# Kernel tuning notes

Measured on AMD Instinct MI355X. Metric: run time of the kernel, lower is better.

Reference implementation:

```python
import jax, jax.numpy as jnp
import numpy as np

B, V, D, K, C_IN, C_OUT = 64, 2000, 16, 3, 64, 64


def setup_inputs() -> dict:
    key = jax.random.key(0)
    ks = jax.random.split(key, 7)
    return {
        "x": jax.random.normal(ks[0], (B, V, C_IN), dtype=jnp.float32),
        "ne_re": jax.random.normal(ks[1], (V, D), dtype=jnp.float32),
        "ne_im": jax.random.normal(ks[2], (V, D), dtype=jnp.float32),
        "w_re": jax.random.normal(ks[3], (D, K, C_IN, C_OUT), dtype=jnp.float32),
        "w_im": jax.random.normal(ks[4], (D, K, C_IN, C_OUT), dtype=jnp.float32),
        "b_re": jax.random.normal(ks[5], (D, C_OUT), dtype=jnp.float32),
        "b_im": jax.random.normal(ks[6], (D, C_OUT), dtype=jnp.float32),
    }


def reference(x, ne_re, ne_im, w_re, w_im, b_re, b_im):
    # Complex node embeddings and parameter pools (param_type='complex').
    ne = jax.lax.complex(ne_re, ne_im)                      # (V, D) complex64
    w_pool = jax.lax.complex(w_re, w_im)                    # (D, K, Ci, Co)
    b_pool = jax.lax.complex(b_re, b_im)                    # (D, Co)

    # Laplacian = E E^H, Frobenius-normalized (activation=None, normalization='frob').
    lap = ne @ ne.conj().T                                  # (V, V)
    lap = lap / jnp.linalg.norm(lap)

    # Node-adaptive weights and bias.
    weights = jnp.einsum('vd,dkio->vkio', ne, w_pool)       # (V, K, Ci, Co)
    bias = ne @ b_pool                                      # (V, Co)

    # Chebyshev-style recurrence, faithful to the source: T_k = 2*T_{k-1} - T_{k-2}
    # (the original code omits the laplacian matmul in the recurrence).
    polys = [jnp.eye(V, dtype=lap.dtype), lap]
    for k in range(2, K):
        polys.append(2.0 * polys[k - 1] - polys[k - 2])
    cheb = jnp.stack(polys, axis=0)                         # (K, V, V)

    xc = x.astype(lap.dtype)                                # (B, V, Ci)
    gx = jnp.einsum('kuv,bvi->buki', cheb, xc)              # (B, V, K, Ci)
    out = jnp.einsum('bvki,vkio->bvo', gx, weights) + bias  # (B, V, Co) complex

    # unwind=True path: view_as_real + flatten(2,3) -> interleaved (re, im).
    return jnp.stack([out.real, out.imag], axis=-1).reshape(B, V, 2 * C_OUT)
```

## Files before the change

### kernel.cpp

```cpp
#include <hip/hip_runtime.h>
#include <stdint.h>

#define BB 64
#define VV 2000
#define DD 16
#define CI 64
#define CO 64

#define WS_INV_DW   0
#define WS_Z_DW     1024
#define WS_BIAS_DW  132096
#define WS_NE_B     1552384UL
#define WS_RHS_B    1814528UL
#define WS_U_B      4960256UL
#define WS_W_B      54112256UL
#define WS_ZP_DW    33554432
#define WS_NP_DW    (WS_ZP_DW + 2097152)

typedef __attribute__((ext_vector_type(8))) short short8;
typedef __attribute__((ext_vector_type(4))) float f32x4;

__device__ __forceinline__ uint32_t f2bf(float f) {
  uint32_t u = __float_as_uint(f);
  return (u + 0x7FFFu + ((u >> 16) & 1u)) >> 16;
}

__device__ __forceinline__ void gload_lds16(const void* g, void* l) {
  __builtin_amdgcn_global_load_lds(
      (const __attribute__((address_space(1))) uint32_t*)g,
      (__attribute__((address_space(3))) uint32_t*)l, 16, 0, 0);
}


__device__ __forceinline__ void body_z(int bz, int t,
    const float* __restrict__ x, const float* __restrict__ ne_re,
    const float* __restrict__ ne_im, float* __restrict__ ws) {
  int b = bz >> 4, c = bz & 15;
  int lane = t & 63;
  int w = __builtin_amdgcn_readfirstlane(t >> 6);
  __shared__ __align__(16) float smem[8192];

  int vbase = c * 125;

  {
    const float4* xg = (const float4*)(x + ((size_t)b * VV + vbase) * CI);
    int wb = t & 192;
    #pragma unroll
    for (int p = 0; p < 8; ++p) {
      int idx = p * 256 + t;
      if (idx < 2000)
        gload_lds16(xg + idx, &smem[(p * 256 + wb) * 4]);
    }
  }
  __syncthreads();

  float zr[DD], zi[DD];
  #pragma unroll
  for (int d = 0; d < DD; ++d) { zr[d] = 0.f; zi[d] = 0.f; }

  uint16_t* Ux = (uint16_t*)((char*)ws + WS_U_B);
  int bkey = b & 7;
  int pos = (((lane >> 3) ^ bkey) & 7)*8 + (lane & 7);

  int lv0 = (w * 125) >> 2;
  int lv1 = ((w + 1) * 125) >> 2;
  #pragma unroll 4
  for (int lv = lv0; lv < lv1; ++lv) {
    float xv = smem[lv * 64 + lane];
    int v = vbase + lv;
    Ux[(size_t)v*12288 + b*64 + pos] = (uint16_t)f2bf(xv);
    #pragma unroll
    for (int d = 0; d < DD; ++d) {
      zr[d] += ne_re[v*DD + d] * xv;
      zi[d] -= ne_im[v*DD + d] * xv;
    }
  }
  __syncthreads();

  #pragma unroll
  for (int d = 0; d < DD; ++d) {
    smem[w*2048 + d*128 + lane*2 + 0] = zr[d];
    smem[w*2048 + d*128 + lane*2 + 1] = zi[d];
  }
  __syncthreads();
  float* ZP = ws + WS_ZP_DW;
  #pragma unroll
  for (int k = 0; k < 8; ++k) {
    int j = t + k*256;
    float s = smem[j] + smem[2048 + j] + smem[4096 + j] + smem[6144 + j];
    int d = j >> 7, r = j & 127;
    ZP[(size_t)c*131072 + d*8192 + b*128 + r] = s;
  }
}

__device__ __forceinline__ void body_ne(int bx, int t,
    const float* __restrict__ ne_re, const float* __restrict__ ne_im,
    float* __restrict__ ws) {
  int gid = bx * 256 + t;
  int u = gid >> 6, col = gid & 63;
  int h = col >> 5, kk = col & 31, d = kk >> 1, p = kk & 1;
  float v = 0.f;
  if (u < VV) v = p ? ne_im[u*DD + d] : ne_re[u*DD + d];
  uint32_t hi = f2bf(v);
  uint32_t ov = h ? f2bf(v - __uint_as_float(hi << 16)) : hi;
  ((uint16_t*)((char*)ws + WS_NE_B))[gid] = (uint16_t)ov;
}

__device__ __forceinline__ void body_rhs(int bx, int t,
    const float* __restrict__ w_re, const float* __restrict__ w_im,
    float* __restrict__ ws) {
  int c = bx >> 6, sub = bx & 63;
  int ig4 = sub & 15, dq = sub >> 4;
  int o = t & 63, il = t >> 6;
  int i = ig4*4 + il;
  int cb = c >> 1;
  int imf = c & 1;

  uint32_t row32[4];
  #pragma unroll
  for (int d4 = 0; d4 < 4; ++d4) {
    int d = dq*4 + d4;
    int b0 = (d*192 + i)*64 + o;
    float vre, vim;
    if (cb == 0) {
      vre = w_re[b0] - w_re[b0 + 8192];
      vim = w_im[b0] - w_im[b0 + 8192];
    } else {
      vre = w_re[b0 + 4096] + 2.f*w_re[b0 + 8192];
      vim = w_im[b0 + 4096] + 2.f*w_im[b0 + 8192];
    }
    float q0 = imf ? vim : vre;
    float q1 = imf ? vre : -vim;
    row32[d4] = f2bf(q0) | (f2bf(q1) << 16);
  }
  int s = ((i >> 3) ^ (o & 7)) & 7;
  int n = c*4096 + o*64 + s*8 + (i & 7);
  uint4* dst = (uint4*)((uint16_t*)((char*)ws + WS_RHS_B) + (size_t)n*64);
  uint4 qv = make_uint4(row32[0], row32[1], row32[2], row32[3]);
  dst[dq]     = qv;
  dst[dq + 4] = qv;
}

__device__ __forceinline__ void body_norm1(int bx, int t,
    const float* __restrict__ ne_re, const float* __restrict__ ne_im,
    float* __restrict__ ws) {
  int d = t >> 4, e = t & 15;
  int v0 = bx * 20;
  float gr = 0.f, gi = 0.f;
  #pragma unroll 4
  for (int v = v0; v < v0 + 20; ++v) {
    float ar = ne_re[v*DD + d], ai = ne_im[v*DD + d];
    float br = ne_re[v*DD + e], bi = ne_im[v*DD + e];
    gr += ar*br + ai*bi;
    gi += ar*bi - ai*br;
  }
  float* NP = ws + WS_NP_DW;
  NP[bx*512 + 2*t]     = gr;
  NP[bx*512 + 2*t + 1] = gi;
}

__device__ __forceinline__ void body_bias(int bx, int t,
    const float* __restrict__ ne_re, const float* __restrict__ ne_im,
    const float* __restrict__ b_re, const float* __restrict__ b_im,
    float* __restrict__ ws) {
  int gid = bx * 256 + t;
  int u = gid >> 7, idx = gid & 127;
  int o = idx >> 1, half = idx & 1;
  float acc = 0.f;
  #pragma unroll
  for (int d = 0; d < DD; ++d) {
    float nr = ne_re[u*DD + d], ni = ne_im[u*DD + d];
    float pr = b_re[d*CO + o],  pi = b_im[d*CO + o];
    acc += half ? (nr*pi + ni*pr) : (nr*pr - ni*pi);
  }
  ws[WS_BIAS_DW + gid] = acc;
}

__device__ __forceinline__ void body_wgemm(int bx, int t, float* __restrict__ ws) {
  const uint16_t* NE  = (const uint16_t*)((char*)ws + WS_NE_B);
  const uint16_t* RHS = (const uint16_t*)((char*)ws + WS_RHS_B);
  uint32_t*       W   = (uint32_t*)((char*)ws + WS_W_B);
  int ut = bx & 31, nc = bx >> 5;
  int w = t >> 6, lane = t & 63;
  int n16 = lane & 15, quad = lane >> 4;
  short8 a[4][2];
  #pragma unroll
  for (int m = 0; m < 4; ++m) {
    int u = ut*64 + m*16 + n16;
    a[m][0] = *(const short8*)(NE + u*64 + quad*8);
    a[m][1] = *(const short8*)(NE + u*64 + 32 + quad*8);
  }
  int nbase = nc*1024 + w*256;
  #pragma unroll 2
  for (int pt = 0; pt < 8; ++pt) {
    int nb = nbase + pt*32;
    const uint16_t* r0 = RHS + (size_t)(nb + 2*n16 + 0)*64 + quad*8;
    const uint16_t* r1 = RHS + (size_t)(nb + 2*n16 + 1)*64 + quad*8;
    short8 b00 = *(const short8*)r0;
    short8 b01 = *(const short8*)(r0 + 32);
    short8 b10 = *(const short8*)r1;
    short8 b11 = *(const short8*)(r1 + 32);
    #pragma unroll
    for (int m = 0; m < 4; ++m) {
      f32x4 acc0 = (f32x4){0.f,0.f,0.f,0.f};
      f32x4 acc1 = (f32x4){0.f,0.f,0.f,0.f};
      acc0 = __builtin_amdgcn_mfma_f32_16x16x32_bf16(a[m][0], b00, acc0, 0, 0, 0);
      acc0 = __builtin_amdgcn_mfma_f32_16x16x32_bf16(a[m][1], b01, acc0, 0, 0, 0);
      acc1 = __builtin_amdgcn_mfma_f32_16x16x32_bf16(a[m][0], b10, acc1, 0, 0, 0);
      acc1 = __builtin_amdgcn_mfma_f32_16x16x32_bf16(a[m][1], b11, acc1, 0, 0, 0);
      #pragma unroll
      for (int r = 0; r < 4; ++r) {
        int u = ut*64 + m*16 + quad*4 + r;
        if (u < VV) {
          uint32_t pk = f2bf(acc0[r]) | (f2bf(acc1[r]) << 16);
          W[(size_t)u*8192 + (nb >> 1) + n16] = pk;
        }
      }
    }
  }
}

__device__ __forceinline__ void body_zred(int bx, int t, float* __restrict__ ws) {
  int g = bx * 256 + t;
  const float2* ZP2 = (const float2*)(ws + WS_ZP_DW);
  float2 acc = make_float2(0.f, 0.f);
  #pragma unroll
  for (int c = 0; c < 16; ++c) {
    float2 v = ZP2[(size_t)c*65536 + g];
    acc.x += v.x; acc.y += v.y;
  }
  ((float2*)(ws + WS_Z_DW))[g] = acc;
}

__device__ __forceinline__ void body_norm2(int t, float* __restrict__ ws) {
  const float* NP = ws + WS_NP_DW;
  float gr = 0.f, gi = 0.f;
  #pragma unroll
  for (int p = 0; p < 100; ++p) {
    gr += NP[p*512 + 2*t];
    gi += NP[p*512 + 2*t + 1];
  }
  __shared__ float red[256];
  red[t] = gr*gr + gi*gi;
  __syncthreads();
  for (int k = 128; k > 0; k >>= 1) {
    if (t < k) red[t] += red[t + k];
    __syncthreads();
  }
  if (t == 0) ws[WS_INV_DW] = 1.0f / sqrtf(red[0]);
}


__global__ void __launch_bounds__(256, 4)
k_front(const float* __restrict__ x, const float* __restrict__ ne_re,
        const float* __restrict__ ne_im, const float* __restrict__ w_re,
        const float* __restrict__ w_im, const float* __restrict__ b_re,
        const float* __restrict__ b_im, float* __restrict__ ws) {
  int bx = blockIdx.x, t = threadIdx.x;
  if (bx < 1024) {
    body_z(bx, t, x, ne_re, ne_im, ws);
  } else if (bx < 1280) {
    body_rhs(bx - 1024, t, w_re, w_im, ws);
  } else if (bx < 1380) {
    body_norm1(bx - 1280, t, ne_re, ne_im, ws);
  } else if (bx < 2380) {
    body_bias(bx - 1380, t, ne_re, ne_im, b_re, b_im, ws);
  } else {
    body_ne(bx - 2380, t, ne_re, ne_im, ws);
  }
}

__global__ void __launch_bounds__(256, 4)
k_mid(float* __restrict__ ws) {
  int bx = blockIdx.x, t = threadIdx.x;
  if (bx < 512) {
    body_wgemm(bx, t, ws);
  } else if (bx < 768) {
    body_zred(bx - 512, t, ws);
  } else {
    body_norm2(t, ws);
  }
}

__global__ void __launch_bounds__(256, 4)
k_u(const float* __restrict__ x, const float* __restrict__ ne_re,
    const float* __restrict__ ne_im, float* __restrict__ ws) {
  (void)x;
  int ug = blockIdx.x, by = blockIdx.y;
  int t = threadIdx.x, q = t >> 6, i = t & 63;
  int b = by*4 + q;
  float invn = ws[WS_INV_DW];

  const float* Z = ws + WS_Z_DW;
  float zr[DD], zi[DD];
  #pragma unroll
  for (int d = 0; d < DD; ++d) {
    const float* zp = Z + (size_t)(d*4096 + b*64 + i) * 2;
    zr[d] = zp[0]; zi[d] = zp[1];
  }

  __shared__ uint16_t sStage[128 * 64];
  int bkey = b & 7;
  int pos = (((i >> 3) ^ bkey) & 7)*8 + (i & 7);

  #pragma unroll
  for (int ul = 0; ul < 16; ++ul) {
    int u = ug*16 + ul;
    float yra = 0.f, yrb = 0.f, yia = 0.f, yib = 0.f;
    #pragma unroll
    for (int d = 0; d < DD; ++d) {
      float nr = ne_re[u*DD + d], ni = ne_im[u*DD + d];
      yra += nr*zr[d]; yrb += ni*zi[d];
      yia += nr*zi[d]; yib += ni*zr[d];
    }
    float yr = yra - yrb, yi = yia + yib;
    sStage[(ul*8 + 0 + q)*64 + pos] = (uint16_t)f2bf(yr * invn);
    sStage[(ul*8 + 4 + q)*64 + pos] = (uint16_t)f2bf(yi * invn);
  }
  __syncthreads();
  uint16_t* U = (uint16_t*)((char*)ws + WS_U_B);
  const uint4* sv = (const uint4*)sStage;
  #pragma unroll
  for (int pass = 0; pass < 4; ++pass) {
    int rr = pass*32 + (t >> 3), l8 = t & 7;
    int ul = rr >> 3, rem = rr & 7;
    int cc = rem >> 2, qq = rem & 3;
    uint4 v = sv[rr*8 + l8];
    *(uint4*)(U + (size_t)(ug*16 + ul)*12288 + (1+cc)*4096 + (by*4 + qq)*64 + l8*8) = v;
  }
}

#define LP 80
#define CSTRIDE 5120
__global__ void __launch_bounds__(512, 2)
k_final(const float* __restrict__ ws, float* __restrict__ out) {
  int u = blockIdx.x, t = threadIdx.x;
  __shared__ __align__(16) uint16_t sW[4 * CSTRIDE];
  __shared__ __align__(16) uint16_t sU[3 * CSTRIDE];
  const uint4* Wg = (const uint4*)((const char*)ws + WS_W_B + (size_t)u*32768);
  const uint4* Ug = (const uint4*)((const char*)ws + WS_U_B + (size_t)u*24576);
  #pragma unroll
  for (int j = 0; j < 4; ++j) {
    int idx = j*512 + t;
    int row = idx >> 3, col = idx & 7;
    *(uint4*)&sW[row*LP + col*8] = Wg[idx];
  }
  #pragma unroll
  for (int j = 0; j < 3; ++j) {
    int idx = j*512 + t;
    int row = idx >> 3, col = idx & 7;
    *(uint4*)&sU[row*LP + col*8] = Ug[idx];
  }
  __syncthreads();

  int w = t >> 6, lane = t & 63;
  int n16 = lane & 15, quad = lane >> 4;
  int o = w*8 + (n16 >> 1), half = n16 & 1;
  int okey = o & 7;
  uint32_t sgnmask = half ? 0u : 0x80008000u;
  f32x4 acc[4];
  #pragma unroll
  for (int m = 0; m < 4; ++m) acc[m] = (f32x4){0.f,0.f,0.f,0.f};

  #pragma unroll
  for (int ks = 0; ks < 6; ++ks) {
    int cb = ks >> 1;
    int i8 = (ks & 1)*4 + quad;
    int c  = (cb == 0) ? half : ((cb == 1) ? 2 + half : 3 - half);
    int slot = (i8 ^ okey) & 7;
    short8 bfrag = *(const short8*)&sW[c*CSTRIDE + o*LP + slot*8];
    if (cb == 2) {
      uint32_t* bu = (uint32_t*)&bfrag;
      #pragma unroll
      for (int jj = 0; jj < 4; ++jj) bu[jj] ^= sgnmask;
    }
    #pragma unroll
    for (int m = 0; m < 4; ++m) {
      int b = m*16 + n16;
      int aslot = (i8 ^ (b & 7)) & 7;
      short8 afrag = *(const short8*)&sU[cb*CSTRIDE + b*LP + aslot*8];
      acc[m] = __builtin_amdgcn_mfma_f32_16x16x32_bf16(afrag, bfrag, acc[m], 0, 0, 0);
    }
  }

  float bias = ws[WS_BIAS_DW + u*128 + w*16 + n16];
  #pragma unroll
  for (int m = 0; m < 4; ++m) {
    #pragma unroll
    for (int r = 0; r < 4; ++r) {
      int b = m*16 + quad*4 + r;
      out[((size_t)b*VV + u)*128 + w*16 + n16] = acc[m][r] + bias;
    }
  }
}

extern "C" void kernel_launch(void* const* d_in, const int* in_sizes, int n_in,
                              void* d_out, int out_size, void* d_ws, size_t ws_size,
                              hipStream_t stream) {
  (void)in_sizes; (void)n_in; (void)out_size; (void)ws_size;
  const float* x     = (const float*)d_in[0];
  const float* ne_re = (const float*)d_in[1];
  const float* ne_im = (const float*)d_in[2];
  const float* w_re  = (const float*)d_in[3];
  const float* w_im  = (const float*)d_in[4];
  const float* b_re  = (const float*)d_in[5];
  const float* b_im  = (const float*)d_in[6];
  float* out = (float*)d_out;
  float* ws  = (float*)d_ws;

  k_front<<<dim3(2892),    dim3(256), 0, stream>>>(x, ne_re, ne_im, w_re, w_im,
                                                   b_re, b_im, ws);
  k_mid  <<<dim3(769),     dim3(256), 0, stream>>>(ws);
  k_u    <<<dim3(125, 16), dim3(256), 0, stream>>>(x, ne_re, ne_im, ws);
  k_final<<<dim3(VV),      dim3(512), 0, stream>>>(ws, out);
}
```

Measured before the change: 179.9 us.

## Stage k_final operands through registers into a smaller shared buffer in two phases

k_final now loads all W and U tiles from global into registers first, then writes them to a single shared buffer of 256 rows in two phases: the cb=0 slice is computed, then the buffer is overwritten with the remaining slices. This roughly halves LDS use per block, and the launch bound goes from 2 to 6 blocks per SM so more blocks can be resident and hide the global load latency. The cost is an extra barrier pair and the register pressure of holding seven uint4 values per thread.

```diff
diff --git a/kernel.cpp b/kernel.cpp
--- a/kernel.cpp
+++ b/kernel.cpp
@@ -332,26 +332,18 @@
 
 #define LP 80
 #define CSTRIDE 5120
-__global__ void __launch_bounds__(512, 2)
+__global__ void __launch_bounds__(512, 6)
 k_final(const float* __restrict__ ws, float* __restrict__ out) {
   int u = blockIdx.x, t = threadIdx.x;
-  __shared__ __align__(16) uint16_t sW[4 * CSTRIDE];
-  __shared__ __align__(16) uint16_t sU[3 * CSTRIDE];
+  __shared__ __align__(16) uint16_t sB[256 * LP];
   const uint4* Wg = (const uint4*)((const char*)ws + WS_W_B + (size_t)u*32768);
   const uint4* Ug = (const uint4*)((const char*)ws + WS_U_B + (size_t)u*24576);
-  #pragma unroll
-  for (int j = 0; j < 4; ++j) {
-    int idx = j*512 + t;
-    int row = idx >> 3, col = idx & 7;
-    *(uint4*)&sW[row*LP + col*8] = Wg[idx];
-  }
-  #pragma unroll
-  for (int j = 0; j < 3; ++j) {
-    int idx = j*512 + t;
-    int row = idx >> 3, col = idx & 7;
-    *(uint4*)&sU[row*LP + col*8] = Ug[idx];
-  }
-  __syncthreads();
+
+  uint4 rW[4], rU[3];
+  #pragma unroll
+  for (int j = 0; j < 4; ++j) rW[j] = Wg[j*512 + t];
+  #pragma unroll
+  for (int j = 0; j < 3; ++j) rU[j] = Ug[j*512 + t];
 
   int w = t >> 6, lane = t & 63;
   int n16 = lane & 15, quad = lane >> 4;
@@ -363,22 +355,65 @@
   for (int m = 0; m < 4; ++m) acc[m] = (f32x4){0.f,0.f,0.f,0.f};
 
   #pragma unroll
-  for (int ks = 0; ks < 6; ++ks) {
+  for (int j = 0; j < 2; ++j) {
+    int idx = j*512 + t;
+    *(uint4*)&sB[(idx >> 3)*LP + (idx & 7)*8] = rW[j];
+  }
+  {
+    int idx = t;
+    *(uint4*)&sB[(128 + (idx >> 3))*LP + (idx & 7)*8] = rU[0];
+  }
+  __syncthreads();
+
+  #pragma unroll
+  for (int ks = 0; ks < 2; ++ks) {
+    int i8 = ks*4 + quad;
+    int c  = half;
+    int slot = (i8 ^ okey) & 7;
+    short8 bfrag = *(const short8*)&sB[c*CSTRIDE + o*LP + slot*8];
+    #pragma unroll
+    for (int m = 0; m < 4; ++m) {
+      int b = m*16 + n16;
+      int aslot = (i8 ^ (b & 7)) & 7;
+      short8 afrag = *(const short8*)&sB[(128 + b)*LP + aslot*8];
+      acc[m] = __builtin_amdgcn_mfma_f32_16x16x32_bf16(afrag, bfrag, acc[m], 0, 0, 0);
+    }
+  }
+  __syncthreads();
+
+  #pragma unroll
+  for (int j = 2; j < 4; ++j) {
+    int idx = j*512 + t;
+    int row = (idx >> 3) - 128;
+    *(uint4*)&sB[row*LP + (idx & 7)*8] = rW[j];
+  }
+  #pragma unroll
+  for (int j = 1; j < 3; ++j) {
+    int idx = j*512 + t;
+    int row = (idx >> 3) - 64;
+    *(uint4*)&sB[(128 + row)*LP + (idx & 7)*8] = rU[j];
+  }
+  __syncthreads();
+
+  #pragma unroll
+  for (int ks = 2; ks < 6; ++ks) {
     int cb = ks >> 1;
     int i8 = (ks & 1)*4 + quad;
-    int c  = (cb == 0) ? half : ((cb == 1) ? 2 + half : 3 - half);
+    int c  = (cb == 1) ? 2 + half : 3 - half;
+    int c2 = c - 2;
     int slot = (i8 ^ okey) & 7;
-    short8 bfrag = *(const short8*)&sW[c*CSTRIDE + o*LP + slot*8];
+    short8 bfrag = *(const short8*)&sB[c2*CSTRIDE + o*LP + slot*8];
     if (cb == 2) {
       uint32_t* bu = (uint32_t*)&bfrag;
       #pragma unroll
       for (int jj = 0; jj < 4; ++jj) bu[jj] ^= sgnmask;
     }
+    int cbl = cb - 1;
     #pragma unroll
     for (int m = 0; m < 4; ++m) {
       int b = m*16 + n16;
       int aslot = (i8 ^ (b & 7)) & 7;
-      short8 afrag = *(const short8*)&sU[cb*CSTRIDE + b*LP + aslot*8];
+      short8 afrag = *(const short8*)&sB[(128 + cbl*64 + b)*LP + aslot*8];
       acc[m] = __builtin_amdgcn_mfma_f32_16x16x32_bf16(afrag, bfrag, acc[m], 0, 0, 0);
     }
   }
```

Result: slower. 222.8 us (+23.8%).
